# Optimization experiments

Hardware: AMD Instinct MI355X
Metric: run time of the kernel (lower is better)

The kernel has to match this reference:

```python
import jax, jax.numpy as jnp
import numpy as np

N_COARSE = 64
N_FINE = 64  # n_fine_depth = 0
HIDDEN = 128
R = 16384


def setup_inputs() -> dict:
    key = jax.random.key(0)
    ks = jax.random.split(key, 8)
    origins = jax.random.normal(ks[0], (R, 3), dtype=jnp.float32)
    dirs = jax.random.normal(ks[1], (R, 3), dtype=jnp.float32)
    dirs = dirs / jnp.linalg.norm(dirs, axis=-1, keepdims=True)
    near = jnp.full((R, 1), 2.0, dtype=jnp.float32)
    far = jnp.full((R, 1), 6.0, dtype=jnp.float32)
    rays = jnp.concatenate([origins, dirs, near, far], axis=-1)  # [R, 8]
    u_coarse = jax.random.uniform(ks[2], (R, N_COARSE), dtype=jnp.float32)
    u_fine = jax.random.uniform(ks[3], (R, N_FINE), dtype=jnp.float32)
    u_jitter = jax.random.uniform(ks[4], (R, N_FINE), dtype=jnp.float32)
    W1 = jax.random.normal(ks[5], (3, HIDDEN), dtype=jnp.float32) * 0.5
    b1 = jnp.zeros((HIDDEN,), dtype=jnp.float32)
    W2 = jax.random.normal(ks[6], (HIDDEN, 4), dtype=jnp.float32) * 0.1
    b2 = jnp.zeros((4,), dtype=jnp.float32)
    return dict(rays=rays, u_coarse=u_coarse, u_fine=u_fine, u_jitter=u_jitter,
                W1=W1, b1=b1, W2=W2, b2=b2)


def _mlp(pts, W1, b1, W2, b2):
    # pts: [R, K, 3] -> [R, K, 4] (r, g, b, sigma)
    h = jax.nn.relu(pts @ W1 + b1)
    return h @ W2 + b2


def _composite(rays, z_sample, W1, b1, W2, b2):
    # z_sample: [R, K]; faithful to NeRFRenderer.composite
    deltas = jnp.concatenate(
        [z_sample[:, 1:] - z_sample[:, :-1], rays[:, 7:8] - z_sample[:, -1:]], axis=-1)
    pts = rays[:, None, :3] + z_sample[..., None] * rays[:, None, 3:6]  # [R, K, 3]
    out = _mlp(pts, W1, b1, W2, b2)
    rgbs = out[..., :3]
    sigmas = out[..., 3]
    alphas = 1.0 - jnp.exp(-deltas * jax.nn.relu(sigmas))
    alphas_shifted = jnp.concatenate(
        [jnp.ones_like(alphas[:, :1]), 1.0 - alphas + 1e-10], axis=-1)
    T = jnp.cumprod(alphas_shifted, axis=-1)
    weights = alphas * T[:, :-1]  # [R, K]
    rgb_final = jnp.sum(weights[..., None] * rgbs, axis=-2)  # [R, 3]
    depth_final = jnp.sum(weights * z_sample, axis=-1)       # [R]
    return weights, rgb_final, depth_final


def reference(rays, u_coarse, u_fine, u_jitter, W1, b1, W2, b2):
    near, far = rays[:, 6:7], rays[:, 7:8]
    # ---- coarse stratified sampling ----
    step = 1.0 / N_COARSE
    z_steps = jnp.linspace(0.0, 1.0 - step, N_COARSE, dtype=jnp.float32)[None, :] \
        + u_coarse * step
    z_coarse = near * (1.0 - z_steps) + far * z_steps  # [R, Kc] (lindisp=False)
    w_c, rgb_c, depth_c = _composite(rays, z_coarse, W1, b1, W2, b2)
    # ---- fine importance sampling (inverse CDF on detached coarse weights) ----
    w = jax.lax.stop_gradient(w_c) + 1e-5
    pdf = w / jnp.sum(w, axis=-1, keepdims=True)
    cdf = jnp.cumsum(pdf, axis=-1)
    cdf = jnp.concatenate([jnp.zeros_like(cdf[:, :1]), cdf], axis=-1)  # [R, Kc+1]
    inds = jax.vmap(lambda c, u: jnp.searchsorted(c, u, side='right'))(cdf, u_fine)
    inds = jnp.maximum(inds.astype(jnp.float32) - 1.0, 0.0)
    zf_steps = (inds + u_jitter) / N_COARSE
    z_fine = near * (1.0 - zf_steps) + far * zf_steps  # [R, Kf]
    z_all = jnp.sort(jnp.concatenate([z_coarse, z_fine], axis=-1), axis=-1)  # [R, Kc+Kf]
    w_f, rgb_f, depth_f = _composite(rays, z_all, W1, b1, W2, b2)
    # pack outputs: [R, 8] = [coarse rgb(3), coarse depth(1), fine rgb(3), fine depth(1)]
    return jnp.concatenate(
        [rgb_c, depth_c[:, None], rgb_f, depth_f[:, None]], axis=-1)
```

## Files before the change

### kernel.cpp

```cpp
#include <hip/hip_runtime.h>

#define HID 128

typedef _Float16 f16x8 __attribute__((ext_vector_type(8)));
typedef _Float16 f16x2 __attribute__((ext_vector_type(2)));
typedef float f32x4 __attribute__((ext_vector_type(4)));

union HV { f16x8 v; f16x2 h[4]; };

template <int CTRL, int RM = 0xF, int BM = 0xF>
__device__ __forceinline__ float updf(float old, float src) {
    int o = __builtin_bit_cast(int, old);
    int s = __builtin_bit_cast(int, src);
    int r = __builtin_amdgcn_update_dpp(o, s, CTRL, RM, BM, false);
    return __builtin_bit_cast(float, r);
}

__device__ __forceinline__ float readlanef(float v, int l) {
    return __builtin_bit_cast(float, __builtin_amdgcn_readlane(__builtin_bit_cast(int, v), l));
}

__device__ __forceinline__ float dscan_add(float v) {
    v += updf<0x111>(0.0f, v);
    v += updf<0x112>(0.0f, v);
    v += updf<0x114>(0.0f, v);
    v += updf<0x118>(0.0f, v);
    v += updf<0x142, 0xA>(0.0f, v);
    v += updf<0x143, 0xC>(0.0f, v);
    return v;
}

__device__ __forceinline__ float dscan_mul(float v) {
    v *= updf<0x111>(1.0f, v);
    v *= updf<0x112>(1.0f, v);
    v *= updf<0x114>(1.0f, v);
    v *= updf<0x118>(1.0f, v);
    v *= updf<0x142, 0xA>(1.0f, v);
    v *= updf<0x143, 0xC>(1.0f, v);
    return v;
}

__device__ __forceinline__ float dexcl(float incl, float ident) {
    return updf<0x138>(ident, incl);
}
__device__ __forceinline__ float dnext(float v) {
    return updf<0x130>(0.0f, v);
}

template <int IMM>
__device__ __forceinline__ float swzf(float v) {
    return __builtin_bit_cast(float,
        __builtin_amdgcn_ds_swizzle(__builtin_bit_cast(int, v), IMM));
}

template <int M>
__device__ __forceinline__ float bx(float v) {
    if constexpr (M == 1)       return updf<0xB1>(v, v);
    else if constexpr (M == 2)  return updf<0x4E>(v, v);
    else if constexpr (M == 4)  return swzf<0x101F>(v);
    else if constexpr (M == 8)  return swzf<0x201F>(v);
    else if constexpr (M == 16) return swzf<0x401F>(v);
    else                        return __shfl_xor(v, 32, 64);
}

__device__ __forceinline__ HV cvt8(const float* __restrict__ p) {
    const float4 lo = *(const float4*)p;
    const float4 hi = *(const float4*)(p + 4);
    HV u;
    u.h[0] = f16x2{ (_Float16)lo.x, (_Float16)lo.y };
    u.h[1] = f16x2{ (_Float16)lo.z, (_Float16)lo.w };
    u.h[2] = f16x2{ (_Float16)hi.x, (_Float16)hi.y };
    u.h[3] = f16x2{ (_Float16)hi.z, (_Float16)hi.w };
    return u;
}

__device__ __forceinline__ f32x4 selg(f32x4 a, f32x4 b, f32x4 c, f32x4 d, int g) {
    f32x4 r = a;
    r = (g == 1) ? b : r;
    r = (g == 2) ? c : r;
    r = (g == 3) ? d : r;
    return r;
}

__device__ __forceinline__ f32x4 mlp_tile(float x, float y, float z,
                                          const HV rw0[4], const HV rw1[4],
                                          const HV rw2[4], const HV rb[4],
                                          const f16x8 w2t[4], f32x4 C) {
    const _Float16 xs = (_Float16)x, ys = (_Float16)y, zs = (_Float16)z;
    const f16x2 xp = { xs, xs };
    const f16x2 yp = { ys, ys };
    const f16x2 zp = { zs, zs };
    const f16x2 zero2 = { (_Float16)0, (_Float16)0 };
#pragma unroll
    for (int c = 0; c < 4; ++c) {
        HV hb;
#pragma unroll
        for (int r = 0; r < 4; ++r) {
            f16x2 acc = rw0[c].h[r] * xp + rb[c].h[r];
            acc = rw1[c].h[r] * yp + acc;
            acc = rw2[c].h[r] * zp + acc;
            hb.h[r] = __builtin_elementwise_max(acc, zero2);
        }
        C = __builtin_amdgcn_mfma_f32_16x16x32_f16(w2t[c], hb.v, C, 0, 0, 0);
    }
    return C;
}

extern "C" __global__ void __launch_bounds__(256)
nerf_fused(const float* __restrict__ rays,
           const float* __restrict__ u_coarse,
           const float* __restrict__ u_fine,
           const float* __restrict__ u_jitter,
           const float* __restrict__ W1,
           const float* __restrict__ b1,
           const float* __restrict__ W2,
           const float* __restrict__ b2,
           float* __restrict__ out) {
    const int lane = threadIdx.x & 63;
    const int wv   = threadIdx.x >> 6;
    const int ray  = (blockIdx.x << 2) + wv;
    const int s16  = lane & 15;
    const int g    = lane >> 4;

    __shared__ float s_cdf[4][65];
    __shared__ float s_zc [4][64];
    __shared__ float s_zf [4][64];
    __shared__ float s_za [4][130];

    HV rw0[4], rw1[4], rw2[4], rb[4];
#pragma unroll
    for (int c = 0; c < 4; ++c) {
        const int hid0 = 32 * c + 8 * g;
        rw0[c] = cvt8(W1 + hid0);
        rw1[c] = cvt8(W1 + HID + hid0);
        rw2[c] = cvt8(W1 + 2 * HID + hid0);
        rb [c] = cvt8(b1 + hid0);
    }
    f16x8 w2t[4];
#pragma unroll
    for (int c = 0; c < 4; ++c) {
        HV u;
#pragma unroll
        for (int r = 0; r < 4; ++r) {
            const int k0 = 32 * c + 8 * g + 2 * r;
            const float a0 = W2[k0 * 4 + (s16 & 3)];
            const float a1 = W2[(k0 + 1) * 4 + (s16 & 3)];
            u.h[r] = f16x2{ (_Float16)a0, (_Float16)a1 };
        }
        w2t[c] = u.v;
    }
    f32x4 cini;
    cini[0] = b2[0]; cini[1] = b2[1]; cini[2] = b2[2]; cini[3] = b2[3];

    const float* rp = rays + ray * 8;
    const float ox = rp[0], oy = rp[1], oz = rp[2];
    const float dx = rp[3], dy = rp[4], dz = rp[5];
    const float nearv = rp[6], farv = rp[7];

    const float uc = u_coarse[(ray << 6) + lane];
    const float zsv = ((float)lane + uc) * 0.015625f;
    const float zc = nearv * (1.0f - zsv) + farv * zsv;
    s_zc[wv][lane] = zc;

    float zt[4];
#pragma unroll
    for (int t = 0; t < 4; ++t) zt[t] = s_zc[wv][t * 16 + s16];
    f32x4 C0, C1, C2, C3;
    {
        C0 = mlp_tile(fmaf(zt[0], dx, ox), fmaf(zt[0], dy, oy), fmaf(zt[0], dz, oz), rw0, rw1, rw2, rb, w2t, cini);
        C1 = mlp_tile(fmaf(zt[1], dx, ox), fmaf(zt[1], dy, oy), fmaf(zt[1], dz, oz), rw0, rw1, rw2, rb, w2t, cini);
        C2 = mlp_tile(fmaf(zt[2], dx, ox), fmaf(zt[2], dy, oy), fmaf(zt[2], dz, oz), rw0, rw1, rw2, rb, w2t, cini);
        C3 = mlp_tile(fmaf(zt[3], dx, ox), fmaf(zt[3], dy, oy), fmaf(zt[3], dz, oz), rw0, rw1, rw2, rb, w2t, cini);
    }
    const f32x4 cv = selg(C0, C1, C2, C3, g);

    {
        const float znext = dnext(zc);
        const float delta = (lane == 63) ? (farv - zc) : (znext - zc);
        const float alpha = 1.0f - __expf(-delta * fmaxf(cv[3], 0.0f));

        const float f  = 1.0f - alpha + 1e-10f;
        const float ip = dscan_mul(f);
        const float Te = dexcl(ip, 1.0f);
        const float w  = alpha * Te;

        const float rS = dscan_add(w * cv[0]);
        const float gS = dscan_add(w * cv[1]);
        const float bS = dscan_add(w * cv[2]);
        const float dS = dscan_add(w * zc);

        const float wp = w + 1e-5f;
        const float cs = dscan_add(wp);
        const float total = readlanef(cs, 63);
        if (lane == 0) s_cdf[wv][0] = 0.0f;
        s_cdf[wv][lane + 1] = cs / total;

        if (lane == 63) {
            float4* op = (float4*)(out + ray * 8);
            op[0] = make_float4(rS, gS, bS, dS);
        }
    }

    const float uf = u_fine[(ray << 6) + lane];
    const float uj = u_jitter[(ray << 6) + lane];

    int lo = 0, hi = 65;
#pragma unroll
    for (int it = 0; it < 7; ++it) {
        if (lo < hi) {
            int mid = (lo + hi) >> 1;
            if (s_cdf[wv][mid] <= uf) lo = mid + 1; else hi = mid;
        }
    }
    const float ind = fmaxf((float)lo - 1.0f, 0.0f);
    const float zfs = (ind + uj) * 0.015625f;
    const float zfv = nearv * (1.0f - zfs) + farv * zfs;

    float v = zfv;
#define BSTEP(K, J) { float o = bx<J>(v);                               \
                      bool asc = ((lane & K) == 0);                     \
                      bool low = ((lane & J) == 0);                     \
                      float mn = fminf(v, o), mx = fmaxf(v, o);         \
                      v = (asc == low) ? mn : mx; }
    BSTEP(2, 1)
    BSTEP(4, 2)  BSTEP(4, 1)
    BSTEP(8, 4)  BSTEP(8, 2)  BSTEP(8, 1)
    BSTEP(16, 8) BSTEP(16, 4) BSTEP(16, 2) BSTEP(16, 1)
    BSTEP(32, 16) BSTEP(32, 8) BSTEP(32, 4) BSTEP(32, 2) BSTEP(32, 1)
    BSTEP(64, 32) BSTEP(64, 16) BSTEP(64, 8) BSTEP(64, 4) BSTEP(64, 2) BSTEP(64, 1)
#undef BSTEP
    s_zf[wv][lane] = v;

    int lof = 0, hif = 64;
#pragma unroll
    for (int it = 0; it < 7; ++it) {
        if (lof < hif) {
            int mid = (lof + hif) >> 1;
            if (s_zf[wv][mid] < zc) lof = mid + 1; else hif = mid;
        }
    }
    int loc = 0, hic = 64;
#pragma unroll
    for (int it = 0; it < 7; ++it) {
        if (loc < hic) {
            int mid = (loc + hic) >> 1;
            if (s_zc[wv][mid] <= v) loc = mid + 1; else hic = mid;
        }
    }
    s_za[wv][lane + lof] = zc;
    s_za[wv][lane + loc] = v;

    float zu[8];
#pragma unroll
    for (int t = 0; t < 8; ++t) zu[t] = s_za[wv][t * 16 + s16];

    f32x4 vA, vB;
    {
        f32x4 F0 = mlp_tile(fmaf(zu[0], dx, ox), fmaf(zu[0], dy, oy), fmaf(zu[0], dz, oz), rw0, rw1, rw2, rb, w2t, cini);
        f32x4 F1 = mlp_tile(fmaf(zu[1], dx, ox), fmaf(zu[1], dy, oy), fmaf(zu[1], dz, oz), rw0, rw1, rw2, rb, w2t, cini);
        f32x4 F2 = mlp_tile(fmaf(zu[2], dx, ox), fmaf(zu[2], dy, oy), fmaf(zu[2], dz, oz), rw0, rw1, rw2, rb, w2t, cini);
        f32x4 F3 = mlp_tile(fmaf(zu[3], dx, ox), fmaf(zu[3], dy, oy), fmaf(zu[3], dz, oz), rw0, rw1, rw2, rb, w2t, cini);
        vA = selg(F0, F1, F2, F3, g);
    }
    {
        f32x4 F4 = mlp_tile(fmaf(zu[4], dx, ox), fmaf(zu[4], dy, oy), fmaf(zu[4], dz, oz), rw0, rw1, rw2, rb, w2t, cini);
        f32x4 F5 = mlp_tile(fmaf(zu[5], dx, ox), fmaf(zu[5], dy, oy), fmaf(zu[5], dz, oz), rw0, rw1, rw2, rb, w2t, cini);
        f32x4 F6 = mlp_tile(fmaf(zu[6], dx, ox), fmaf(zu[6], dy, oy), fmaf(zu[6], dz, oz), rw0, rw1, rw2, rb, w2t, cini);
        f32x4 F7 = mlp_tile(fmaf(zu[7], dx, ox), fmaf(zu[7], dy, oy), fmaf(zu[7], dz, oz), rw0, rw1, rw2, rb, w2t, cini);
        vB = selg(F4, F5, F6, F7, g);
    }

    {
        const float zA = s_za[wv][lane];
        const float zB = s_za[wv][lane + 64];

        const float zA1 = dnext(zA);
        const float zB1 = dnext(zB);
        const float zB0 = readlanef(zB, 0);
        const float dA = (lane == 63) ? (zB0 - zA) : (zA1 - zA);
        const float dB = (lane == 63) ? (farv - zB) : (zB1 - zB);

        const float aA = 1.0f - __expf(-dA * fmaxf(vA[3], 0.0f));
        const float aB = 1.0f - __expf(-dB * fmaxf(vB[3], 0.0f));
        const float fA = 1.0f - aA + 1e-10f;
        const float fB = 1.0f - aB + 1e-10f;

        const float ipA = dscan_mul(fA);
        const float TA  = dexcl(ipA, 1.0f);
        const float wA  = aA * TA;

        const float Pall = readlanef(ipA, 63);
        const float ipB = dscan_mul(fB);
        const float TBp = dexcl(ipB, 1.0f);
        const float wB  = aB * Pall * TBp;

        const float rS = dscan_add(fmaf(wA, vA[0], wB * vB[0]));
        const float gS = dscan_add(fmaf(wA, vA[1], wB * vB[1]));
        const float bS = dscan_add(fmaf(wA, vA[2], wB * vB[2]));
        const float dS = dscan_add(fmaf(wA, zA, wB * zB));

        if (lane == 63) {
            float4* op = (float4*)(out + ray * 8);
            op[1] = make_float4(rS, gS, bS, dS);
        }
    }
}

extern "C" void kernel_launch(void* const* d_in, const int* in_sizes, int n_in,
                              void* d_out, int out_size, void* d_ws, size_t ws_size,
                              hipStream_t stream) {
    const float* rays = (const float*)d_in[0];
    const float* uc   = (const float*)d_in[1];
    const float* uf   = (const float*)d_in[2];
    const float* uj   = (const float*)d_in[3];
    const float* W1   = (const float*)d_in[4];
    const float* b1   = (const float*)d_in[5];
    const float* W2   = (const float*)d_in[6];
    const float* b2   = (const float*)d_in[7];
    float* o          = (float*)d_out;

    const int R = in_sizes[0] / 8;
    dim3 grid(R / 4), block(256);
    hipLaunchKernelGGL(nerf_fused, grid, block, 0, stream,
                       rays, uc, uf, uj, W1, b1, W2, b2, o);
}
```

Before: 127.8 us.

## Fold ray origin and direction into per-ray first-layer coefficients

Each ray's origin and direction are folded into the first MLP layer once per ray, precomputing P = o·W1 + b1 and Q = d·W1. Each hidden activation is then a single packed fp16 FMA in z instead of three FMAs plus a bias, and the 16 register arrays drop to 8. The output bias is added after the MFMA chain instead of seeding the accumulator, tile selection is done incrementally to cut live registers, and launch bounds now request higher occupancy. Rounding P and Q to fp16 before the z-multiply changes numerics slightly, since the fp16 z·Q product can differ from computing the point in fp32.

```diff
diff --git a/kernel.cpp b/kernel.cpp
--- a/kernel.cpp
+++ b/kernel.cpp
@@ -63,42 +63,23 @@
     else                        return __shfl_xor(v, 32, 64);
 }
 
-__device__ __forceinline__ HV cvt8(const float* __restrict__ p) {
-    const float4 lo = *(const float4*)p;
-    const float4 hi = *(const float4*)(p + 4);
-    HV u;
-    u.h[0] = f16x2{ (_Float16)lo.x, (_Float16)lo.y };
-    u.h[1] = f16x2{ (_Float16)lo.z, (_Float16)lo.w };
-    u.h[2] = f16x2{ (_Float16)hi.x, (_Float16)hi.y };
-    u.h[3] = f16x2{ (_Float16)hi.z, (_Float16)hi.w };
-    return u;
-}
-
-__device__ __forceinline__ f32x4 selg(f32x4 a, f32x4 b, f32x4 c, f32x4 d, int g) {
-    f32x4 r = a;
-    r = (g == 1) ? b : r;
-    r = (g == 2) ? c : r;
-    r = (g == 3) ? d : r;
-    return r;
-}
-
-__device__ __forceinline__ f32x4 mlp_tile(float x, float y, float z,
-                                          const HV rw0[4], const HV rw1[4],
-                                          const HV rw2[4], const HV rb[4],
-                                          const f16x8 w2t[4], f32x4 C) {
-    const _Float16 xs = (_Float16)x, ys = (_Float16)y, zs = (_Float16)z;
-    const f16x2 xp = { xs, xs };
-    const f16x2 yp = { ys, ys };
-    const f16x2 zp = { zs, zs };
+__device__ __forceinline__ f16x2 pk2(float a, float b) {
+    return f16x2{ (_Float16)a, (_Float16)b };
+}
+
+__device__ __forceinline__ f32x4 mlp_tile(float zf,
+                                          const HV P[4], const HV Q[4],
+                                          const f16x8 w2t[4]) {
+    const _Float16 zh = (_Float16)zf;
+    const f16x2 zp = { zh, zh };
     const f16x2 zero2 = { (_Float16)0, (_Float16)0 };
+    f32x4 C = { 0.0f, 0.0f, 0.0f, 0.0f };
 #pragma unroll
     for (int c = 0; c < 4; ++c) {
         HV hb;
 #pragma unroll
         for (int r = 0; r < 4; ++r) {
-            f16x2 acc = rw0[c].h[r] * xp + rb[c].h[r];
-            acc = rw1[c].h[r] * yp + acc;
-            acc = rw2[c].h[r] * zp + acc;
+            f16x2 acc = Q[c].h[r] * zp + P[c].h[r];
             hb.h[r] = __builtin_elementwise_max(acc, zero2);
         }
         C = __builtin_amdgcn_mfma_f32_16x16x32_f16(w2t[c], hb.v, C, 0, 0, 0);
@@ -106,7 +87,7 @@
     return C;
 }
 
-extern "C" __global__ void __launch_bounds__(256)
+extern "C" __global__ void __launch_bounds__(256, 8)
 nerf_fused(const float* __restrict__ rays,
            const float* __restrict__ u_coarse,
            const float* __restrict__ u_fine,
@@ -127,15 +108,36 @@
     __shared__ float s_zf [4][64];
     __shared__ float s_za [4][130];
 
-    HV rw0[4], rw1[4], rw2[4], rb[4];
+    const float* rp = rays + ray * 8;
+    const float ox = rp[0], oy = rp[1], oz = rp[2];
+    const float dx = rp[3], dy = rp[4], dz = rp[5];
+    const float nearv = rp[6], farv = rp[7];
+
+    HV P[4], Q[4];
 #pragma unroll
     for (int c = 0; c < 4; ++c) {
         const int hid0 = 32 * c + 8 * g;
-        rw0[c] = cvt8(W1 + hid0);
-        rw1[c] = cvt8(W1 + HID + hid0);
-        rw2[c] = cvt8(W1 + 2 * HID + hid0);
-        rb [c] = cvt8(b1 + hid0);
-    }
+        const float* w0p = W1 + hid0;
+        const float* w1p = W1 + HID + hid0;
+        const float* w2p = W1 + 2 * HID + hid0;
+        const float* bp  = b1 + hid0;
+        HV Pv, Qv;
+#pragma unroll
+        for (int r = 0; r < 4; ++r) {
+            const float a0 = w0p[2 * r], a1 = w0p[2 * r + 1];
+            const float e0 = w1p[2 * r], e1 = w1p[2 * r + 1];
+            const float c0 = w2p[2 * r], c1 = w2p[2 * r + 1];
+            const float f0 = bp [2 * r], f1 = bp [2 * r + 1];
+            const float p0 = fmaf(ox, a0, fmaf(oy, e0, fmaf(oz, c0, f0)));
+            const float p1 = fmaf(ox, a1, fmaf(oy, e1, fmaf(oz, c1, f1)));
+            const float q0 = fmaf(dx, a0, fmaf(dy, e0, dz * c0));
+            const float q1 = fmaf(dx, a1, fmaf(dy, e1, dz * c1));
+            Pv.h[r] = pk2(p0, p1);
+            Qv.h[r] = pk2(q0, q1);
+        }
+        P[c] = Pv; Q[c] = Qv;
+    }
+
     f16x8 w2t[4];
 #pragma unroll
     for (int c = 0; c < 4; ++c) {
@@ -145,34 +147,25 @@
             const int k0 = 32 * c + 8 * g + 2 * r;
             const float a0 = W2[k0 * 4 + (s16 & 3)];
             const float a1 = W2[(k0 + 1) * 4 + (s16 & 3)];
-            u.h[r] = f16x2{ (_Float16)a0, (_Float16)a1 };
+            u.h[r] = pk2(a0, a1);
         }
         w2t[c] = u.v;
     }
-    f32x4 cini;
-    cini[0] = b2[0]; cini[1] = b2[1]; cini[2] = b2[2]; cini[3] = b2[3];
-
-    const float* rp = rays + ray * 8;
-    const float ox = rp[0], oy = rp[1], oz = rp[2];
-    const float dx = rp[3], dy = rp[4], dz = rp[5];
-    const float nearv = rp[6], farv = rp[7];
+    const float b2s0 = b2[0], b2s1 = b2[1], b2s2 = b2[2], b2s3 = b2[3];
 
     const float uc = u_coarse[(ray << 6) + lane];
     const float zsv = ((float)lane + uc) * 0.015625f;
     const float zc = nearv * (1.0f - zsv) + farv * zsv;
     s_zc[wv][lane] = zc;
 
-    float zt[4];
-#pragma unroll
-    for (int t = 0; t < 4; ++t) zt[t] = s_zc[wv][t * 16 + s16];
-    f32x4 C0, C1, C2, C3;
-    {
-        C0 = mlp_tile(fmaf(zt[0], dx, ox), fmaf(zt[0], dy, oy), fmaf(zt[0], dz, oz), rw0, rw1, rw2, rb, w2t, cini);
-        C1 = mlp_tile(fmaf(zt[1], dx, ox), fmaf(zt[1], dy, oy), fmaf(zt[1], dz, oz), rw0, rw1, rw2, rb, w2t, cini);
-        C2 = mlp_tile(fmaf(zt[2], dx, ox), fmaf(zt[2], dy, oy), fmaf(zt[2], dz, oz), rw0, rw1, rw2, rb, w2t, cini);
-        C3 = mlp_tile(fmaf(zt[3], dx, ox), fmaf(zt[3], dy, oy), fmaf(zt[3], dz, oz), rw0, rw1, rw2, rb, w2t, cini);
-    }
-    const f32x4 cv = selg(C0, C1, C2, C3, g);
+    f32x4 cv;
+#pragma unroll
+    for (int t = 0; t < 4; ++t) {
+        const float ztv = s_zc[wv][t * 16 + s16];
+        const f32x4 Ct = mlp_tile(ztv, P, Q, w2t);
+        cv = (t == 0) ? Ct : ((g == t) ? Ct : cv);
+    }
+    cv[0] += b2s0; cv[1] += b2s1; cv[2] += b2s2; cv[3] += b2s3;
 
     {
         const float znext = dnext(zc);
@@ -250,25 +243,22 @@
     s_za[wv][lane + lof] = zc;
     s_za[wv][lane + loc] = v;
 
-    float zu[8];
-#pragma unroll
-    for (int t = 0; t < 8; ++t) zu[t] = s_za[wv][t * 16 + s16];
-
-    f32x4 vA, vB;
-    {
-        f32x4 F0 = mlp_tile(fmaf(zu[0], dx, ox), fmaf(zu[0], dy, oy), fmaf(zu[0], dz, oz), rw0, rw1, rw2, rb, w2t, cini);
-        f32x4 F1 = mlp_tile(fmaf(zu[1], dx, ox), fmaf(zu[1], dy, oy), fmaf(zu[1], dz, oz), rw0, rw1, rw2, rb, w2t, cini);
-        f32x4 F2 = mlp_tile(fmaf(zu[2], dx, ox), fmaf(zu[2], dy, oy), fmaf(zu[2], dz, oz), rw0, rw1, rw2, rb, w2t, cini);
-        f32x4 F3 = mlp_tile(fmaf(zu[3], dx, ox), fmaf(zu[3], dy, oy), fmaf(zu[3], dz, oz), rw0, rw1, rw2, rb, w2t, cini);
-        vA = selg(F0, F1, F2, F3, g);
-    }
-    {
-        f32x4 F4 = mlp_tile(fmaf(zu[4], dx, ox), fmaf(zu[4], dy, oy), fmaf(zu[4], dz, oz), rw0, rw1, rw2, rb, w2t, cini);
-        f32x4 F5 = mlp_tile(fmaf(zu[5], dx, ox), fmaf(zu[5], dy, oy), fmaf(zu[5], dz, oz), rw0, rw1, rw2, rb, w2t, cini);
-        f32x4 F6 = mlp_tile(fmaf(zu[6], dx, ox), fmaf(zu[6], dy, oy), fmaf(zu[6], dz, oz), rw0, rw1, rw2, rb, w2t, cini);
-        f32x4 F7 = mlp_tile(fmaf(zu[7], dx, ox), fmaf(zu[7], dy, oy), fmaf(zu[7], dz, oz), rw0, rw1, rw2, rb, w2t, cini);
-        vB = selg(F4, F5, F6, F7, g);
-    }
+    f32x4 vA;
+#pragma unroll
+    for (int t = 0; t < 4; ++t) {
+        const float ztv = s_za[wv][t * 16 + s16];
+        const f32x4 Ct = mlp_tile(ztv, P, Q, w2t);
+        vA = (t == 0) ? Ct : ((g == t) ? Ct : vA);
+    }
+    f32x4 vB;
+#pragma unroll
+    for (int t = 0; t < 4; ++t) {
+        const float ztv = s_za[wv][64 + t * 16 + s16];
+        const f32x4 Ct = mlp_tile(ztv, P, Q, w2t);
+        vB = (t == 0) ? Ct : ((g == t) ? Ct : vB);
+    }
+    vA[0] += b2s0; vA[1] += b2s1; vA[2] += b2s2; vA[3] += b2s3;
+    vB[0] += b2s0; vB[1] += b2s1; vB[2] += b2s2; vB[3] += b2s3;
 
     {
         const float zA = s_za[wv][lane];
```

Result: slower. 232.2 us (+81.6%).
